# Performance work log

Measured on AMD Instinct MI355X. Metric: run time of the kernel, lower is better.

Reference implementation:

```python
import jax, jax.numpy as jnp
import numpy as np

N_NODES = 100000
N_EDGES = 1600000
D = 64


def gcn_conv(x, src, dst, W, b, n_nodes):
    # x: [N, Din] -> linear first (as GCNConv does), then normalized aggregation
    x = x @ W  # [N, Dout]
    ones = jnp.ones((src.shape[0],), dtype=x.dtype)
    # degree including self-loop (GCN adds self loops with weight 1)
    deg = jax.ops.segment_sum(ones, dst, num_segments=n_nodes) + 1.0
    dinv = jax.lax.rsqrt(deg)
    norm = dinv[src] * dinv[dst]  # [E]
    msgs = x[src] * norm[:, None]  # [E, Dout] gathered messages
    agg = jax.ops.segment_sum(msgs, dst, num_segments=n_nodes)
    # self-loop contribution: norm_ii = deg_i^-1
    agg = agg + x * (1.0 / deg)[:, None]
    return agg + b


def setup_inputs() -> dict:
    key = jax.random.key(0)
    k1, k2, k3, k4 = jax.random.split(key, 4)
    feature = jax.random.normal(k1, (N_NODES, D), dtype=jnp.float32)
    edge_index = jax.random.randint(k2, (2, N_EDGES), 0, N_NODES, dtype=jnp.int64)
    scale = float(np.sqrt(6.0 / (D + D)))  # xavier_uniform bound
    W1 = jax.random.uniform(k3, (D, D), dtype=jnp.float32, minval=-scale, maxval=scale)
    W2 = jax.random.uniform(k4, (D, D), dtype=jnp.float32, minval=-scale, maxval=scale)
    b1 = jnp.zeros((D,), dtype=jnp.float32)
    b2 = jnp.zeros((D,), dtype=jnp.float32)
    return {"feature": feature, "edge_index": edge_index,
            "W1": W1, "b1": b1, "W2": W2, "b2": b2}


def reference(feature, edge_index, W1, b1, W2, b2):
    # baseGNN.forward iterates convs[:-1]; with num_layers=3 -> 2 convs applied.
    # Dropout is identity in eval mode (training=False).
    src, dst = edge_index[0], edge_index[1]
    x = gcn_conv(feature, src, dst, W1, b1, N_NODES)
    x = jax.nn.relu(x)
    x = gcn_conv(x, src, dst, W2, b2, N_NODES)
    x = jax.nn.relu(x)
    return x
```

## Files before the change

kernel.cpp:

```cpp
#include <hip/hip_runtime.h>
#include <hip/hip_fp16.h>

#define N_NODES 100000
#define N_EDGES 1600000
#define D 64

#define NB 256
#define BUCKET_W 391
#define NB_USED 256
#define NBLK 256
#define CHUNK ((N_EDGES + NBLK - 1) / NBLK)
#define CCAP 7168
#define LMASK 511

__global__ __launch_bounds__(1024) void partition_fused(const int* __restrict__ src,
                                                        const int* __restrict__ dst,
                                                        int* __restrict__ cursor,
                                                        int* __restrict__ part) {
    __shared__ int h[NB];
    __shared__ int lcur[NB];
    const int t = threadIdx.x;
    if (t < NB) h[t] = 0;
    __syncthreads();
    const int blk = blockIdx.x;
    const int beg = blk * CHUNK;
    const int end = min(beg + CHUNK, N_EDGES);
    for (int e = beg + t; e < end; e += 1024)
        atomicAdd(&h[dst[e] / BUCKET_W], 1);
    __syncthreads();
    if (t < NB) {
        const int c = h[t];
        const int base = c ? atomicAdd(&cursor[t * 16], c) : 0;
        lcur[t] = t * CCAP + base;
    }
    __syncthreads();
    for (int e = beg + t; e < end; e += 1024) {
        const int d = dst[e];
        const int s = src[e];
        const int b = d / BUCKET_W;
        const int pos = atomicAdd(&lcur[b], 1);
        part[pos] = (s << 9) | (d - b * BUCKET_W);
    }
}

__global__ __launch_bounds__(512) void bucket_csr(const int* __restrict__ cursor,
                                                  const int* __restrict__ part,
                                                  const float* __restrict__ feature,
                                                  int* __restrict__ col,
                                                  int2* __restrict__ rows,
                                                  float* __restrict__ dinv,
                                                  __half* __restrict__ xh) {
    __shared__ int ed[CCAP];
    __shared__ int hist[BUCKET_W];
    __shared__ int lcur[BUCKET_W];
    __shared__ int sc[512];
    const int b = blockIdx.x;
    const int base = b * CCAP;
    const int cnt = min(cursor[b * 16], CCAP);
    const int n0 = b * BUCKET_W;
    const int nn = min(N_NODES - n0, BUCKET_W);
    const int t = threadIdx.x;

    if (t < BUCKET_W) hist[t] = 0;
    for (int i = t; i < cnt; i += 512) ed[i] = part[base + i];
    __syncthreads();
    for (int i = t; i < cnt; i += 512) atomicAdd(&hist[ed[i] & LMASK], 1);
    __syncthreads();
    const int v = (t < nn) ? hist[t] : 0;
    sc[t] = v;
    __syncthreads();
    for (int off = 1; off < 512; off <<= 1) {
        int u = (t >= off) ? sc[t - off] : 0;
        __syncthreads();
        sc[t] += u;
        __syncthreads();
    }
    if (t < nn) {
        const int excl = sc[t] - v;
        lcur[t] = base + excl;
        rows[n0 + t] = make_int2(base + excl, base + excl + v);
        dinv[n0 + t] = rsqrtf((float)v + 1.0f);
    }
    __syncthreads();
    for (int i = t; i < cnt; i += 512) {
        const int p = ed[i];
        const int pos = atomicAdd(&lcur[p & LMASK], 1);
        col[pos] = p >> 9;
    }
    const float2* f2p = (const float2*)feature;
    __half2* x2 = (__half2*)xh;
    for (int i = t; i < nn * 32; i += 512) {
        const int node = i >> 5, idx = i & 31;
        const float dv = rsqrtf((float)hist[node] + 1.0f);
        const float2 u = f2p[(size_t)(n0 + node) * 32 + idx];
        x2[(size_t)(n0 + node) * 32 + idx] = __floats2half2_rn(u.x * dv, u.y * dv);
    }
}

__device__ __forceinline__ int rlane_i(int v, int l) {
    return __builtin_amdgcn_readlane(v, l);
}

#define GPAIR4(accA, accB, accC, accD, creg, tt)                                   \
    {                                                                              \
        const int sa0 = rlane_i(creg, 2 * (tt) + 0), sb0 = rlane_i(creg, 2 * (tt) + 1); \
        const int sa1 = rlane_i(creg, 2 * (tt) + 2), sb1 = rlane_i(creg, 2 * (tt) + 3); \
        const int sa2 = rlane_i(creg, 2 * (tt) + 4), sb2 = rlane_i(creg, 2 * (tt) + 5); \
        const int sa3 = rlane_i(creg, 2 * (tt) + 6), sb3 = rlane_i(creg, 2 * (tt) + 7); \
        const int s0 = hsel ? sb0 : sa0;                                           \
        const int s1 = hsel ? sb1 : sa1;                                           \
        const int s2 = hsel ? sb2 : sa2;                                           \
        const int s3 = hsel ? sb3 : sa3;                                           \
        const float2 v0 = __half22float2(xh2[(size_t)s0 * 32 + f2]);               \
        const float2 v1 = __half22float2(xh2[(size_t)s1 * 32 + f2]);               \
        const float2 v2 = __half22float2(xh2[(size_t)s2 * 32 + f2]);               \
        const float2 v3 = __half22float2(xh2[(size_t)s3 * 32 + f2]);               \
        accA.x += v0.x; accA.y += v0.y;                                            \
        accB.x += v1.x; accB.y += v1.y;                                            \
        accC.x += v2.x; accC.y += v2.y;                                            \
        accD.x += v3.x; accD.y += v3.y;                                            \
    }

#define GPAIR1(accA, creg, tt)                                                     \
    {                                                                              \
        const int sa = rlane_i(creg, 2 * (tt) + 0), sb = rlane_i(creg, 2 * (tt) + 1);   \
        const int s = hsel ? sb : sa;                                              \
        const float2 v = __half22float2(xh2[(size_t)s * 32 + f2]);                 \
        accA.x += v.x; accA.y += v.y;                                              \
    }

#define GODD(accA, creg, ch)                                                       \
    if ((ch) & 1) {                                                                \
        const int s = rlane_i(creg, (ch) - 1);                                     \
        if (!hsel) {                                                               \
            const float2 v = __half22float2(xh2[(size_t)s * 32 + f2]);             \
            accA.x += v.x; accA.y += v.y;                                          \
        }                                                                          \
    }

__global__ __launch_bounds__(256) void agg_pair(const __half* __restrict__ xh,
                                                const int2* __restrict__ rows,
                                                const int* __restrict__ col,
                                                const float* __restrict__ dinv,
                                                __half* __restrict__ aggh, int n) {
    const int gwave = (blockIdx.x * blockDim.x + threadIdx.x) >> 6;
    const int lane = threadIdx.x & 63;
    const int nd0 = gwave * 2;
    if (nd0 >= n) return;
    const int nd1 = nd0 + 1;
    const int f2 = lane & 31;
    const int hsel = lane >> 5;
    const __half2* xh2 = (const __half2*)xh;

    const int2 r0 = rows[nd0];
    const int2 r1 = rows[nd1];
    const int b0 = r0.x, e0 = r0.y;
    const int b1 = r1.x, e1 = r1.y;

    const int ch0 = min(e0 - b0, 64);
    const int ch1 = min(e1 - b1, 64);
    const int c0 = (lane < ch0) ? col[b0 + lane] : 0;
    const int c1 = (lane < ch1) ? col[b1 + lane] : 0;

    float2 A0 = make_float2(0.f, 0.f), A1 = make_float2(0.f, 0.f);
    float2 A2 = make_float2(0.f, 0.f), A3 = make_float2(0.f, 0.f);
    float2 B0 = make_float2(0.f, 0.f), B1 = make_float2(0.f, 0.f);
    float2 B2 = make_float2(0.f, 0.f), B3 = make_float2(0.f, 0.f);

    const int np0 = ch0 >> 1, np1 = ch1 >> 1;
    const int mm = min(np0, np1) & ~3;
    int t = 0;
    for (; t < mm; t += 4) {
        GPAIR4(A0, A1, A2, A3, c0, t)
        GPAIR4(B0, B1, B2, B3, c1, t)
    }
    int t0 = t, t1 = t;
    for (; t0 + 3 < np0; t0 += 4) GPAIR4(A0, A1, A2, A3, c0, t0)
    for (; t0 < np0; ++t0) GPAIR1(A0, c0, t0)
    GODD(A0, c0, ch0)
    for (; t1 + 3 < np1; t1 += 4) GPAIR4(B0, B1, B2, B3, c1, t1)
    for (; t1 < np1; ++t1) GPAIR1(B0, c1, t1)
    GODD(B0, c1, ch1)

    for (int j = b0 + 64; j < e0; j += 64) {
        const int chunk = min(e0 - j, 64);
        const int c = (lane < chunk) ? col[j + lane] : 0;
        const int np = chunk >> 1;
        int tt = 0;
        for (; tt + 3 < np; tt += 4) GPAIR4(A0, A1, A2, A3, c, tt)
        for (; tt < np; ++tt) GPAIR1(A0, c, tt)
        GODD(A0, c, chunk)
    }
    for (int j = b1 + 64; j < e1; j += 64) {
        const int chunk = min(e1 - j, 64);
        const int c = (lane < chunk) ? col[j + lane] : 0;
        const int np = chunk >> 1;
        int tt = 0;
        for (; tt + 3 < np; tt += 4) GPAIR4(B0, B1, B2, B3, c, tt)
        for (; tt < np; ++tt) GPAIR1(B0, c, tt)
        GODD(B0, c, chunk)
    }

    float2 sA, sB;
    sA.x = (A0.x + A1.x) + (A2.x + A3.x);
    sA.y = (A0.y + A1.y) + (A2.y + A3.y);
    sB.x = (B0.x + B1.x) + (B2.x + B3.x);
    sB.y = (B0.y + B1.y) + (B2.y + B3.y);
    sA.x += __shfl_xor(sA.x, 32, 64);
    sA.y += __shfl_xor(sA.y, 32, 64);
    sB.x += __shfl_xor(sB.x, 32, 64);
    sB.y += __shfl_xor(sB.y, 32, 64);

    if (!hsel) {
        __half2* aggh2 = (__half2*)aggh;
        const float dv0 = dinv[nd0], dv1 = dinv[nd1];
        const float2 self0 = __half22float2(xh2[(size_t)nd0 * 32 + f2]);
        const float2 self1 = __half22float2(xh2[(size_t)nd1 * 32 + f2]);
        aggh2[(size_t)nd0 * 32 + f2] =
            __floats2half2_rn(dv0 * (sA.x + self0.x), dv0 * (sA.y + self0.y));
        aggh2[(size_t)nd1 * 32 + f2] =
            __floats2half2_rn(dv1 * (sB.x + self1.x), dv1 * (sB.y + self1.y));
    }
}

__device__ __forceinline__ float rlane_ff(float v, int l) {
    return __int_as_float(__builtin_amdgcn_readlane(__float_as_int(v), l));
}

template <bool SCALED_HALF_OUT>
__global__ __launch_bounds__(256) void gemm64(const __half* __restrict__ aggh,
                                              const float* __restrict__ W,
                                              const float* __restrict__ bias,
                                              const float* __restrict__ dinv,
                                              float* __restrict__ out,
                                              __half* __restrict__ outh, int n) {
    const int lane = threadIdx.x & 63;
    const int gwave = (blockIdx.x * blockDim.x + threadIdx.x) >> 6;
    const int nwaves = (gridDim.x * blockDim.x) >> 6;
    float wcol[64];
#pragma unroll
    for (int k = 0; k < 64; ++k) wcol[k] = W[k * 64 + lane];
    const float bv = bias[lane];

    for (int nd = gwave; nd < n; nd += nwaves) {
        const float a = __half2float(aggh[(size_t)nd * D + lane]);
        float g0 = 0.f, g1 = 0.f, g2 = 0.f, g3 = 0.f;
#pragma unroll
        for (int k = 0; k < 64; k += 4) {
            g0 = fmaf(rlane_ff(a, k + 0), wcol[k + 0], g0);
            g1 = fmaf(rlane_ff(a, k + 1), wcol[k + 1], g1);
            g2 = fmaf(rlane_ff(a, k + 2), wcol[k + 2], g2);
            g3 = fmaf(rlane_ff(a, k + 3), wcol[k + 3], g3);
        }
        const float r = fmaxf((g0 + g1) + (g2 + g3) + bv, 0.f);
        if (SCALED_HALF_OUT)
            outh[(size_t)nd * D + lane] = __float2half(r * dinv[nd]);
        else
            out[(size_t)nd * D + lane] = r;
    }
}

extern "C" void kernel_launch(void* const* d_in, const int* in_sizes, int n_in,
                              void* d_out, int out_size, void* d_ws, size_t ws_size,
                              hipStream_t stream) {
    const float* feature = (const float*)d_in[0];
    const int*   edges   = (const int*)d_in[1];
    const float* W1      = (const float*)d_in[2];
    const float* b1      = (const float*)d_in[3];
    const float* W2      = (const float*)d_in[4];
    const float* b2      = (const float*)d_in[5];
    float* out = (float*)d_out;

    const int* src = edges;
    const int* dst = edges + N_EDGES;

    char* w = (char*)d_ws;
    int*    cursor = (int*)w;    w += sizeof(int) * (NB * 16);
    int2*   rows   = (int2*)w;   w += sizeof(int2) * (N_NODES);
    float*  dinv   = (float*)w;  w += sizeof(float) * (N_NODES);
    int*    part   = (int*)w;    w += sizeof(int) * (NB * CCAP);
    int*    colA   = (int*)w;    w += sizeof(int) * (NB * CCAP);
    __half* xh     = (__half*)w; w += sizeof(__half) * ((size_t)N_NODES * D);
    __half* y1h    = (__half*)w; w += sizeof(__half) * ((size_t)N_NODES * D);
    __half* aggh   = (__half*)w; w += sizeof(__half) * ((size_t)N_NODES * D);

    hipMemsetAsync(cursor, 0, sizeof(int) * NB * 16, stream);
    partition_fused<<<NBLK, 1024, 0, stream>>>(src, dst, cursor, part);
    bucket_csr<<<NB_USED, 512, 0, stream>>>(cursor, part, feature, colA, rows, dinv, xh);

    const int pair_blocks = (N_NODES / 2 + 3) / 4;

    agg_pair<<<pair_blocks, 256, 0, stream>>>(xh, rows, colA, dinv, aggh, N_NODES);
    gemm64<true><<<2048, 256, 0, stream>>>(aggh, W1, b1, dinv, nullptr, y1h, N_NODES);

    agg_pair<<<pair_blocks, 256, 0, stream>>>(y1h, rows, colA, dinv, aggh, N_NODES);
    gemm64<false><<<2048, 256, 0, stream>>>(aggh, W2, b2, dinv, out, nullptr, N_NODES);
}
```

Baseline: 174.0 us.

## Apply linear transform before aggregation and fuse bias/ReLU into aggregation

Reorders each GCN layer to run the 64x64 transform first (scaled by dinv, stored as half) and then aggregate, matching the reference order. Bias and ReLU move into the aggregation epilogue, and the feature scaling pass leaves bucket_csr. This drops the intermediate aggh buffer and one write/read pass per layer. The cost is that the first GEMM now reads fp32 features directly, and the reordering changes the rounding pattern of the half-precision intermediates.

```diff
diff --git a/kernel.cpp b/kernel.cpp
--- a/kernel.cpp
+++ b/kernel.cpp
@@ -45,11 +45,9 @@
 
 __global__ __launch_bounds__(512) void bucket_csr(const int* __restrict__ cursor,
                                                   const int* __restrict__ part,
-                                                  const float* __restrict__ feature,
                                                   int* __restrict__ col,
                                                   int2* __restrict__ rows,
-                                                  float* __restrict__ dinv,
-                                                  __half* __restrict__ xh) {
+                                                  float* __restrict__ dinv) {
     __shared__ int ed[CCAP];
     __shared__ int hist[BUCKET_W];
     __shared__ int lcur[BUCKET_W];
@@ -87,13 +85,37 @@
         const int pos = atomicAdd(&lcur[p & LMASK], 1);
         col[pos] = p >> 9;
     }
-    const float2* f2p = (const float2*)feature;
-    __half2* x2 = (__half2*)xh;
-    for (int i = t; i < nn * 32; i += 512) {
-        const int node = i >> 5, idx = i & 31;
-        const float dv = rsqrtf((float)hist[node] + 1.0f);
-        const float2 u = f2p[(size_t)(n0 + node) * 32 + idx];
-        x2[(size_t)(n0 + node) * 32 + idx] = __floats2half2_rn(u.x * dv, u.y * dv);
+}
+
+__device__ __forceinline__ float rlane_ff(float v, int l) {
+    return __int_as_float(__builtin_amdgcn_readlane(__float_as_int(v), l));
+}
+
+template <bool IN_HALF>
+__global__ __launch_bounds__(256) void gemm_pre(const void* __restrict__ xin,
+                                                const float* __restrict__ W,
+                                                const float* __restrict__ dinv,
+                                                __half* __restrict__ hsc, int n) {
+    const int lane = threadIdx.x & 63;
+    const int gwave = (blockIdx.x * blockDim.x + threadIdx.x) >> 6;
+    const int nwaves = (gridDim.x * blockDim.x) >> 6;
+    float wcol[64];
+#pragma unroll
+    for (int k = 0; k < 64; ++k) wcol[k] = W[k * 64 + lane];
+
+    for (int nd = gwave; nd < n; nd += nwaves) {
+        float a;
+        if (IN_HALF) a = __half2float(((const __half*)xin)[(size_t)nd * D + lane]);
+        else         a = ((const float*)xin)[(size_t)nd * D + lane];
+        float g0 = 0.f, g1 = 0.f, g2 = 0.f, g3 = 0.f;
+#pragma unroll
+        for (int k = 0; k < 64; k += 4) {
+            g0 = fmaf(rlane_ff(a, k + 0), wcol[k + 0], g0);
+            g1 = fmaf(rlane_ff(a, k + 1), wcol[k + 1], g1);
+            g2 = fmaf(rlane_ff(a, k + 2), wcol[k + 2], g2);
+            g3 = fmaf(rlane_ff(a, k + 3), wcol[k + 3], g3);
+        }
+        hsc[(size_t)nd * D + lane] = __float2half(((g0 + g1) + (g2 + g3)) * dinv[nd]);
     }
 }
 
@@ -138,11 +160,14 @@
         }                                                                          \
     }
 
-__global__ __launch_bounds__(256) void agg_pair(const __half* __restrict__ xh,
+template <bool FINAL>
+__global__ __launch_bounds__(256) void agg_pair(const __half* __restrict__ hsc,
                                                 const int2* __restrict__ rows,
                                                 const int* __restrict__ col,
                                                 const float* __restrict__ dinv,
-                                                __half* __restrict__ aggh, int n) {
+                                                const float* __restrict__ bias,
+                                                float* __restrict__ outf,
+                                                __half* __restrict__ outh, int n) {
     const int gwave = (blockIdx.x * blockDim.x + threadIdx.x) >> 6;
     const int lane = threadIdx.x & 63;
     const int nd0 = gwave * 2;
@@ -150,7 +175,7 @@
     const int nd1 = nd0 + 1;
     const int f2 = lane & 31;
     const int hsel = lane >> 5;
-    const __half2* xh2 = (const __half2*)xh;
+    const __half2* xh2 = (const __half2*)hsc;
 
     const int2 r0 = rows[nd0];
     const int2 r1 = rows[nd1];
@@ -212,51 +237,23 @@
     sB.y += __shfl_xor(sB.y, 32, 64);
 
     if (!hsel) {
-        __half2* aggh2 = (__half2*)aggh;
         const float dv0 = dinv[nd0], dv1 = dinv[nd1];
         const float2 self0 = __half22float2(xh2[(size_t)nd0 * 32 + f2]);
         const float2 self1 = __half22float2(xh2[(size_t)nd1 * 32 + f2]);
-        aggh2[(size_t)nd0 * 32 + f2] =
-            __floats2half2_rn(dv0 * (sA.x + self0.x), dv0 * (sA.y + self0.y));
-        aggh2[(size_t)nd1 * 32 + f2] =
-            __floats2half2_rn(dv1 * (sB.x + self1.x), dv1 * (sB.y + self1.y));
-    }
-}
-
-__device__ __forceinline__ float rlane_ff(float v, int l) {
-    return __int_as_float(__builtin_amdgcn_readlane(__float_as_int(v), l));
-}
-
-template <bool SCALED_HALF_OUT>
-__global__ __launch_bounds__(256) void gemm64(const __half* __restrict__ aggh,
-                                              const float* __restrict__ W,
-                                              const float* __restrict__ bias,
-                                              const float* __restrict__ dinv,
-                                              float* __restrict__ out,
-                                              __half* __restrict__ outh, int n) {
-    const int lane = threadIdx.x & 63;
-    const int gwave = (blockIdx.x * blockDim.x + threadIdx.x) >> 6;
-    const int nwaves = (gridDim.x * blockDim.x) >> 6;
-    float wcol[64];
-#pragma unroll
-    for (int k = 0; k < 64; ++k) wcol[k] = W[k * 64 + lane];
-    const float bv = bias[lane];
-
-    for (int nd = gwave; nd < n; nd += nwaves) {
-        const float a = __half2float(aggh[(size_t)nd * D + lane]);
-        float g0 = 0.f, g1 = 0.f, g2 = 0.f, g3 = 0.f;
-#pragma unroll
-        for (int k = 0; k < 64; k += 4) {
-            g0 = fmaf(rlane_ff(a, k + 0), wcol[k + 0], g0);
-            g1 = fmaf(rlane_ff(a, k + 1), wcol[k + 1], g1);
-            g2 = fmaf(rlane_ff(a, k + 2), wcol[k + 2], g2);
-            g3 = fmaf(rlane_ff(a, k + 3), wcol[k + 3], g3);
+        const float2 bv = *(const float2*)(bias + f2 * 2);
+        const float r0x = fmaxf(fmaf(dv0, sA.x + self0.x, bv.x), 0.f);
+        const float r0y = fmaxf(fmaf(dv0, sA.y + self0.y, bv.y), 0.f);
+        const float r1x = fmaxf(fmaf(dv1, sB.x + self1.x, bv.x), 0.f);
+        const float r1y = fmaxf(fmaf(dv1, sB.y + self1.y, bv.y), 0.f);
+        if (FINAL) {
+            float2* o2 = (float2*)outf;
+            o2[(size_t)nd0 * 32 + f2] = make_float2(r0x, r0y);
+            o2[(size_t)nd1 * 32 + f2] = make_float2(r1x, r1y);
+        } else {
+            __half2* o2 = (__half2*)outh;
+            o2[(size_t)nd0 * 32 + f2] = __floats2half2_rn(r0x, r0y);
+            o2[(size_t)nd1 * 32 + f2] = __floats2half2_rn(r1x, r1y);
         }
-        const float r = fmaxf((g0 + g1) + (g2 + g3) + bv, 0.f);
-        if (SCALED_HALF_OUT)
-            outh[(size_t)nd * D + lane] = __float2half(r * dinv[nd]);
-        else
-            out[(size_t)nd * D + lane] = r;
     }
 }
 
@@ -280,19 +277,20 @@
     float*  dinv   = (float*)w;  w += sizeof(float) * (N_NODES);
     int*    part   = (int*)w;    w += sizeof(int) * (NB * CCAP);
     int*    colA   = (int*)w;    w += sizeof(int) * (NB * CCAP);
-    __half* xh     = (__half*)w; w += sizeof(__half) * ((size_t)N_NODES * D);
+    __half* hsc    = (__half*)w; w += sizeof(__half) * ((size_t)N_NODES * D);
     __half* y1h    = (__half*)w; w += sizeof(__half) * ((size_t)N_NODES * D);
-    __half* aggh   = (__half*)w; w += sizeof(__half) * ((size_t)N_NODES * D);
 
     hipMemsetAsync(cursor, 0, sizeof(int) * NB * 16, stream);
     partition_fused<<<NBLK, 1024, 0, stream>>>(src, dst, cursor, part);
-    bucket_csr<<<NB_USED, 512, 0, stream>>>(cursor, part, feature, colA, rows, dinv, xh);
+    bucket_csr<<<NB_USED, 512, 0, stream>>>(cursor, part, colA, rows, dinv);
 
     const int pair_blocks = (N_NODES / 2 + 3) / 4;
 
-    agg_pair<<<pair_blocks, 256, 0, stream>>>(xh, rows, colA, dinv, aggh, N_NODES);
-    gemm64<true><<<2048, 256, 0, stream>>>(aggh, W1, b1, dinv, nullptr, y1h, N_NODES);
-
-    agg_pair<<<pair_blocks, 256, 0, stream>>>(y1h, rows, colA, dinv, aggh, N_NODES);
-    gemm64<false><<<2048, 256, 0, stream>>>(aggh, W2, b2, dinv, out, nullptr, N_NODES);
-}
+    gemm_pre<false><<<2048, 256, 0, stream>>>(feature, W1, dinv, hsc, N_NODES);
+    agg_pair<false><<<pair_blocks, 256, 0, stream>>>(hsc, rows, colA, dinv, b1,
+                                                     nullptr, y1h, N_NODES);
+
+    gemm_pre<true><<<2048, 256, 0, stream>>>(y1h, W2, dinv, hsc, N_NODES);
+    agg_pair<true><<<pair_blocks, 256, 0, stream>>>(hsc, rows, colA, dinv, b2,
+                                                    out, nullptr, N_NODES);
+}
```

Result: faster. 168.2 us (-3.3%).
